# Optimization experiments

Hardware: AMD Instinct MI355X
Metric: run time of the kernel (lower is better)

The kernel has to match this reference:

```python
import jax, jax.numpy as jnp
import numpy as np

B, C, H, W = 2, 512, 64, 64
HEADS, DHEAD = 8, 64
HID = HEADS * DHEAD  # 512
GROUPS = 32
EPS = 1e-5


def setup_inputs() -> dict:
    key = jax.random.key(0)
    ks = jax.random.split(key, 10)
    w_scale = 0.02
    return {
        "x": jax.random.normal(ks[0], (B, C, H, W), dtype=jnp.float32),
        "gamma": jnp.ones((C,), dtype=jnp.float32),
        "beta": jnp.zeros((C,), dtype=jnp.float32),
        "wq": jax.random.normal(ks[1], (HID, C), dtype=jnp.float32) * w_scale,
        "bq": jax.random.normal(ks[2], (HID,), dtype=jnp.float32) * w_scale,
        "wk": jax.random.normal(ks[3], (HID, C), dtype=jnp.float32) * w_scale,
        "bk": jax.random.normal(ks[4], (HID,), dtype=jnp.float32) * w_scale,
        "wv": jax.random.normal(ks[5], (HID, C), dtype=jnp.float32) * w_scale,
        "bv": jax.random.normal(ks[6], (HID,), dtype=jnp.float32) * w_scale,
        "wo": jax.random.normal(ks[7], (C, HID), dtype=jnp.float32) * w_scale,
        "bo": jax.random.normal(ks[8], (C,), dtype=jnp.float32) * w_scale,
    }


def _group_norm(x, gamma, beta):
    b, c, h, w = x.shape
    xg = x.reshape(b, GROUPS, c // GROUPS, h * w)
    mu = jnp.mean(xg, axis=(2, 3), keepdims=True)
    var = jnp.var(xg, axis=(2, 3), keepdims=True)
    xn = (xg - mu) * jax.lax.rsqrt(var + EPS)
    xn = xn.reshape(b, c, h, w)
    return xn * gamma[None, :, None, None] + beta[None, :, None, None]


def reference(x, gamma, beta, wq, bq, wk, bk, wv, bv, wo, bo):
    b, c, h, w = x.shape
    n = h * w
    # norm + flatten spatial; embedding=None -> self-attention on normed x
    xn = _group_norm(x, gamma, beta).reshape(b, c, n)
    # 1x1 Conv1d projections == channel matmuls
    q = jnp.einsum('oc,bcn->bon', wq, xn) + bq[None, :, None]
    k = jnp.einsum('oc,bcn->bon', wk, xn) + bk[None, :, None]
    v = jnp.einsum('oc,bcn->bon', wv, xn) + bv[None, :, None]
    scale = DHEAD ** (-0.25)  # applied to BOTH q and k, as in source
    qh = q.reshape(b, HEADS, DHEAD, n) * scale
    kh = k.reshape(b, HEADS, DHEAD, n) * scale
    vh = v.reshape(b, HEADS, DHEAD, n)
    # full NxN attention (the materialized score matrix targeted for kernel work)
    attn = jax.nn.softmax(jnp.einsum('bhdi,bhdj->bhij', qh, kh), axis=-1)
    out = jnp.einsum('bhij,bhdj->bhdi', attn, vh).reshape(b, HID, n)
    out = jnp.einsum('oc,bcn->bon', wo, out) + bo[None, :, None]
    out = out.reshape(b, c, h, w)
    return x + out  # in_channels == out_channels -> residual
```

## Files before the change

kernel.cpp:

```cpp
#include <hip/hip_runtime.h>
#include <math.h>

#define BB      2
#define CC      512
#define NN_TOK  4096
#define HEADS   8
#define DHEAD   64
#define HID     512
#define GROUPS  32
#define CPG     (CC / GROUPS)
#define EPS     1e-5f

typedef __bf16 bf16x8 __attribute__((ext_vector_type(8)));
typedef float  f32x4  __attribute__((ext_vector_type(4)));
typedef float  f32x16 __attribute__((ext_vector_type(16)));
typedef int    i32x8  __attribute__((ext_vector_type(8)));

static __device__ __forceinline__ unsigned short f2bf(float f) {
  __bf16 h = (__bf16)f;
  return __builtin_bit_cast(unsigned short, h);
}
static __device__ __forceinline__ float bf2f(unsigned short u) {
  unsigned v = (unsigned)u << 16;
  return __builtin_bit_cast(float, v);
}
static __device__ __forceinline__ unsigned pk_fp8x4(float a, float b, float c, float d) {
  int lo = __builtin_amdgcn_cvt_pk_fp8_f32(a, b, 0, false);
  return (unsigned)__builtin_amdgcn_cvt_pk_fp8_f32(c, d, lo, true);
}
static __device__ __forceinline__ unsigned char f2fp8(float a) {
  return (unsigned char)(__builtin_amdgcn_cvt_pk_fp8_f32(a, a, 0, false) & 0xff);
}
static __device__ __forceinline__ float exp2_fast(float s) {
  float t = __builtin_fmaf(s, 8388608.0f, 1064993216.0f);
  int i = (int)t;
  return __builtin_bit_cast(float, i);
}
static __device__ __forceinline__ i32x8 ld_frag32(const unsigned char* p) {
  union { i32x8 v; long l[4]; } u;
  u.l[0] = *(const long*)(p + 0);
  u.l[1] = *(const long*)(p + 8);
  u.l[2] = *(const long*)(p + 16);
  u.l[3] = *(const long*)(p + 24);
  return u.v;
}
static __device__ __forceinline__ i32x8 ld_g32(const unsigned char* p) {
  union { i32x8 v; uint4 q[2]; } u;
  u.q[0] = *(const uint4*)(p);
  u.q[1] = *(const uint4*)(p + 16);
  return u.v;
}
#define SC_ONE 0x7F7F7F7F
#define QKV_WS 32.0f
#define QKV_WS_INV 0.03125f
#define WO_WS 16.0f
#define WO_WS_INV 0.0625f

__global__ __launch_bounds__(256) void gn_stats_wconv_kernel(
    const float* __restrict__ x, float2* __restrict__ part,
    const float* __restrict__ wq, const float* __restrict__ wk,
    const float* __restrict__ wv, const float* __restrict__ wo,
    unsigned char* __restrict__ wq8, unsigned char* __restrict__ wk8,
    unsigned char* __restrict__ wv8, unsigned char* __restrict__ wo8) {
  int blk = blockIdx.x;
  int t = threadIdx.x;
  {
    int wsel = blk >> 8;
    int off = (blk & 255) * 1024 + t * 4;
    const float* s = (wsel == 0) ? wq : (wsel == 1) ? wk : (wsel == 2) ? wv : wo;
    unsigned char* d = (wsel == 0) ? wq8 : (wsel == 1) ? wk8 : (wsel == 2) ? wv8 : wo8;
    float sc = (wsel < 3) ? QKV_WS : WO_WS;
    float4 a = *(const float4*)&s[off];
    *(unsigned*)&d[off] = pk_fp8x4(a.x * sc, a.y * sc, a.z * sc, a.w * sc);
  }
  const float4* __restrict__ x4 = (const float4*)(x + (size_t)blk * 4096);
  float s = 0.f, ss = 0.f;
  #pragma unroll
  for (int i = 0; i < 4; ++i) {
    float4 v = x4[t + i * 256];
    s  += v.x + v.y + v.z + v.w;
    ss += v.x * v.x + v.y * v.y + v.z * v.z + v.w * v.w;
  }
  #pragma unroll
  for (int off = 32; off >= 1; off >>= 1) {
    s  += __shfl_down(s, off, 64);
    ss += __shfl_down(ss, off, 64);
  }
  __shared__ float rs[4], rss[4];
  int wid = t >> 6, lane = t & 63;
  if (lane == 0) { rs[wid] = s; rss[wid] = ss; }
  __syncthreads();
  if (t == 0) {
    float2 o;
    o.x = rs[0] + rs[1] + rs[2] + rs[3];
    o.y = rss[0] + rss[1] + rss[2] + rss[3];
    part[blk] = o;
  }
}

__global__ __launch_bounds__(256) void gn_norm_t_kernel(
    const float* __restrict__ x, const float* __restrict__ gamma,
    const float* __restrict__ beta, const float2* __restrict__ part,
    unsigned char* __restrict__ xnT8) {
  __shared__ __align__(16) unsigned short lds[64 * 72];
  __shared__ float mu4[4], rs4[4];
  int b = blockIdx.z;
  int t0 = blockIdx.x * 64, c0 = blockIdx.y * 64;
  int t = threadIdx.x;
  if (t < 4) {
    int g = (c0 >> 4) + t;
    int gi = b * GROUPS + g;
    float S = 0.f, SS = 0.f;
    #pragma unroll
    for (int k = 0; k < 16; ++k) {
      float2 p = part[gi * 16 + k];
      S += p.x; SS += p.y;
    }
    const float inv_n = 1.0f / (float)(CPG * NN_TOK);
    float mu = S * inv_n;
    float var = SS * inv_n - mu * mu;
    mu4[t] = mu;
    rs4[t] = rsqrtf(var + EPS);
  }
  __syncthreads();
  const float* __restrict__ xb = x + (size_t)b * CC * NN_TOK;
  #pragma unroll
  for (int i = 0; i < 4; ++i) {
    int f = t + i * 256;
    int row = f >> 4, c16 = f & 15;
    int c = c0 + row;
    float ga = gamma[c] * rs4[row >> 4];
    float be = beta[c] - mu4[row >> 4] * ga;
    float4 v = *(const float4*)&xb[(size_t)c * NN_TOK + t0 + c16 * 4];
    ushort4 pk;
    pk.x = f2bf(v.x * ga + be); pk.y = f2bf(v.y * ga + be);
    pk.z = f2bf(v.z * ga + be); pk.w = f2bf(v.w * ga + be);
    *(ushort4*)&lds[row * 72 + c16 * 4] = pk;
  }
  __syncthreads();
  unsigned char* __restrict__ ob = xnT8 + (size_t)b * NN_TOK * CC;
  #pragma unroll
  for (int i = 0; i < 2; ++i) {
    int f = t + i * 256;
    int row = f >> 3, ch = f & 7;
    float v0 = bf2f(lds[(ch * 8 + 0) * 72 + row]);
    float v1 = bf2f(lds[(ch * 8 + 1) * 72 + row]);
    float v2 = bf2f(lds[(ch * 8 + 2) * 72 + row]);
    float v3 = bf2f(lds[(ch * 8 + 3) * 72 + row]);
    float v4 = bf2f(lds[(ch * 8 + 4) * 72 + row]);
    float v5 = bf2f(lds[(ch * 8 + 5) * 72 + row]);
    float v6 = bf2f(lds[(ch * 8 + 6) * 72 + row]);
    float v7 = bf2f(lds[(ch * 8 + 7) * 72 + row]);
    unsigned lo = pk_fp8x4(v0, v1, v2, v3);
    unsigned hi = pk_fp8x4(v4, v5, v6, v7);
    *(uint2*)&ob[(size_t)(t0 + row) * CC + c0 + ch * 8] = make_uint2(lo, hi);
  }
}

__global__ __launch_bounds__(256, 3) void qkv_gemm_kernel(
    const unsigned char* __restrict__ xnT8,
    const unsigned char* __restrict__ wq8, const unsigned char* __restrict__ wk8,
    const unsigned char* __restrict__ wv8,
    const float* __restrict__ bq, const float* __restrict__ bk,
    const float* __restrict__ bv,
    unsigned char* __restrict__ qT8, unsigned char* __restrict__ kT8,
    unsigned char* __restrict__ vB8) {
  __shared__ __align__(16) unsigned char AB[2][2][128 * 72];
  int b = blockIdx.z;
  int y = blockIdx.y;
  int which = y >> 2, yl = y & 3;
  const unsigned char* __restrict__ W =
      (which == 0) ? wq8 : (which == 1) ? wk8 : wv8;
  const float* __restrict__ bias = (which == 0) ? bq : (which == 1) ? bk : bv;
  int m0 = yl * 128;
  int n0 = blockIdx.x * 128;
  const unsigned char* __restrict__ Bsrc = xnT8 + (size_t)b * NN_TOK * CC;
  int t = threadIdx.x, w = t >> 6, lane = t & 63;
  int wm = (w >> 1) * 64, wn = (w & 1) * 64;
  int l31 = lane & 31, q1h = lane >> 5;

  int sr0 = t >> 2, sr1 = (t + 256) >> 2, sch = t & 3;
  const unsigned char* Wa0 = &W[(size_t)(m0 + sr0) * CC + sch * 16];
  const unsigned char* Wa1 = &W[(size_t)(m0 + sr1) * CC + sch * 16];
  const unsigned char* Bb0 = &Bsrc[(size_t)(n0 + sr0) * CC + sch * 16];
  const unsigned char* Bb1 = &Bsrc[(size_t)(n0 + sr1) * CC + sch * 16];
  uint4 ra0 = *(const uint4*)(Wa0);
  uint4 ra1 = *(const uint4*)(Wa1);
  uint4 rb0 = *(const uint4*)(Bb0);
  uint4 rb1 = *(const uint4*)(Bb1);

  const f32x16 z16 = {0,0,0,0,0,0,0,0,0,0,0,0,0,0,0,0};
  f32x16 acc[2][2];
  #pragma unroll
  for (int mt = 0; mt < 2; ++mt)
    #pragma unroll
    for (int nt = 0; nt < 2; ++nt) acc[mt][nt] = z16;

  int cur = 0;
  for (int kc = 0; kc < CC; kc += 64) {
    __syncthreads();
    {
      unsigned char* As = AB[cur][0];
      unsigned char* Bs = AB[cur][1];
      unsigned char* ad0 = &As[sr0 * 72 + sch * 16];
      *(uint2*)ad0 = make_uint2(ra0.x, ra0.y);
      *(uint2*)(ad0 + 8) = make_uint2(ra0.z, ra0.w);
      unsigned char* ad1 = &As[sr1 * 72 + sch * 16];
      *(uint2*)ad1 = make_uint2(ra1.x, ra1.y);
      *(uint2*)(ad1 + 8) = make_uint2(ra1.z, ra1.w);
      unsigned char* bd0 = &Bs[sr0 * 72 + sch * 16];
      *(uint2*)bd0 = make_uint2(rb0.x, rb0.y);
      *(uint2*)(bd0 + 8) = make_uint2(rb0.z, rb0.w);
      unsigned char* bd1 = &Bs[sr1 * 72 + sch * 16];
      *(uint2*)bd1 = make_uint2(rb1.x, rb1.y);
      *(uint2*)(bd1 + 8) = make_uint2(rb1.z, rb1.w);
    }
    if (kc + 64 < CC) {
      ra0 = *(const uint4*)(Wa0 + kc + 64);
      ra1 = *(const uint4*)(Wa1 + kc + 64);
      rb0 = *(const uint4*)(Bb0 + kc + 64);
      rb1 = *(const uint4*)(Bb1 + kc + 64);
    }
    __syncthreads();
    const unsigned char* As = AB[cur][0];
    const unsigned char* Bs = AB[cur][1];
    i32x8 af[2], bfm[2];
    #pragma unroll
    for (int i = 0; i < 2; ++i) {
      af[i]  = ld_frag32(&As[(wm + i * 32 + l31) * 72 + q1h * 32]);
      bfm[i] = ld_frag32(&Bs[(wn + i * 32 + l31) * 72 + q1h * 32]);
    }
    #pragma unroll
    for (int mt = 0; mt < 2; ++mt)
      #pragma unroll
      for (int nt = 0; nt < 2; ++nt)
        acc[mt][nt] = __builtin_amdgcn_mfma_scale_f32_32x32x64_f8f6f4(
            af[mt], bfm[nt], acc[mt][nt], 0, 0, 0, SC_ONE, 0, SC_ONE);
    cur ^= 1;
  }
  __syncthreads();

  if (which < 2) {
    const float sc = (which == 0) ? 0.18033688011112043f : 1.0f;
    unsigned char* __restrict__ dstT = (which == 0) ? qT8 : kT8;
    unsigned char* buf = (unsigned char*)AB + w * 2560;
    int h = (m0 + wm) >> 6;
    const size_t hbase = (size_t)(b * HEADS + h) * NN_TOK;
    #pragma unroll
    for (int p = 0; p < 2; ++p) {
      #pragma unroll
      for (int mt = 0; mt < 2; ++mt) {
        #pragma unroll
        for (int g = 0; g < 4; ++g) {
          float4 bv4 = *(const float4*)&bias[m0 + wm + mt * 32 + g * 8 + q1h * 4];
          f32x16 a = acc[mt][p];
          unsigned pk = pk_fp8x4((a[4 * g + 0] * QKV_WS_INV + bv4.x) * sc,
                                 (a[4 * g + 1] * QKV_WS_INV + bv4.y) * sc,
                                 (a[4 * g + 2] * QKV_WS_INV + bv4.z) * sc,
                                 (a[4 * g + 3] * QKV_WS_INV + bv4.w) * sc);
          *(unsigned*)&buf[l31 * 80 + mt * 32 + g * 8 + q1h * 4] = pk;
        }
      }
      #pragma unroll
      for (int it = 0; it < 2; ++it) {
        int idx = it * 64 + lane;
        int row = idx >> 2, ch = idx & 3;
        int tok = n0 + wn + p * 32 + row;
        *(uint4*)&dstT[(hbase + tok) * DHEAD + ch * 16] =
            *(const uint4*)&buf[row * 80 + ch * 16];
      }
      __syncthreads();
    }
  } else {
    unsigned char* __restrict__ dst = vB8 + (size_t)b * HID * NN_TOK;
    #pragma unroll
    for (int mt = 0; mt < 2; ++mt) {
      #pragma unroll
      for (int g = 0; g < 4; ++g) {
        float4 bv4 = *(const float4*)&bias[m0 + wm + mt * 32 + g * 8 + q1h * 4];
        float bvr[4] = {bv4.x, bv4.y, bv4.z, bv4.w};
        #pragma unroll
        for (int nt = 0; nt < 2; ++nt) {
          int tok = n0 + wn + nt * 32 + l31;
          #pragma unroll
          for (int r = 0; r < 4; ++r) {
            int m = m0 + wm + mt * 32 + g * 8 + q1h * 4 + r;
            dst[(size_t)m * NN_TOK + tok] =
                f2fp8(acc[mt][nt][4 * g + r] * QKV_WS_INV + bvr[r]);
          }
        }
      }
    }
  }
}

__global__ __launch_bounds__(256) void outproj_kernel(
    const unsigned char* __restrict__ aoT8, const unsigned char* __restrict__ wo8,
    const float* __restrict__ bo, const float* __restrict__ x,
    float* __restrict__ out) {
  __shared__ __align__(16) unsigned char As8[2][64 * 80];
  __shared__ __align__(16) unsigned char Bs8[2][64 * 80];
  int b = blockIdx.z;
  int m0 = blockIdx.y * 64;
  int n0 = blockIdx.x * 64;
  const unsigned char* __restrict__ Bsrc = aoT8 + (size_t)b * NN_TOK * HID;
  int t = threadIdx.x, w = t >> 6, lane = t & 63;
  int wm = (w & 1) * 32, wn = (w >> 1) * 32;
  int l31 = lane & 31, q1h = lane >> 5;

  int ar = t >> 2, ach = t & 3;
  const unsigned char* pa = &wo8[(size_t)(m0 + ar) * HID + ach * 16];
  const unsigned char* pbb = &Bsrc[(size_t)(n0 + ar) * HID + ach * 16];
  uint4 ra = *(const uint4*)(pa);
  uint4 rb = *(const uint4*)(pbb);

  const f32x16 z16 = {0,0,0,0,0,0,0,0,0,0,0,0,0,0,0,0};
  f32x16 acc = z16;

  int cur = 0;
  for (int kc = 0; kc < HID; kc += 64) {
    __syncthreads();
    *(uint4*)&As8[cur][ar * 80 + ach * 16] = ra;
    *(uint4*)&Bs8[cur][ar * 80 + ach * 16] = rb;
    if (kc + 64 < HID) {
      ra = *(const uint4*)(pa + kc + 64);
      rb = *(const uint4*)(pbb + kc + 64);
    }
    __syncthreads();
    i32x8 af = ld_frag32(&As8[cur][(wm + l31) * 80 + q1h * 32]);
    i32x8 bfm = ld_frag32(&Bs8[cur][(wn + l31) * 80 + q1h * 32]);
    acc = __builtin_amdgcn_mfma_scale_f32_32x32x64_f8f6f4(
        af, bfm, acc, 0, 0, 0, SC_ONE, 0, SC_ONE);
    cur ^= 1;
  }

  const float* __restrict__ xb = x + (size_t)b * CC * NN_TOK;
  float* __restrict__ ob = out + (size_t)b * CC * NN_TOK;
  int tok = n0 + wn + l31;
  #pragma unroll
  for (int g = 0; g < 4; ++g) {
    float4 bv4 = *(const float4*)&bo[m0 + wm + g * 8 + q1h * 4];
    float bvr[4] = {bv4.x, bv4.y, bv4.z, bv4.w};
    #pragma unroll
    for (int r = 0; r < 4; ++r) {
      int m = m0 + wm + g * 8 + q1h * 4 + r;
      size_t off = (size_t)m * NN_TOK + tok;
      ob[off] = acc[4 * g + r] * WO_WS_INV + bvr[r] + xb[off];
    }
  }
}

__global__ __launch_bounds__(512, 4) void attn_mfma_kernel(
    const unsigned char* __restrict__ qT8, const unsigned char* __restrict__ kT8,
    const unsigned char* __restrict__ vv8, unsigned char* __restrict__ aoT8) {
  __shared__ __align__(16) unsigned char kvs[2 * 9216];
  __shared__ __align__(16) unsigned char st8[4 * 32 * 80];
  __shared__ float lbuf[128];
  int bh = blockIdx.y;
  int b = bh >> 3, h = bh & 7;
  int i0 = blockIdx.x * 128;
  const size_t hb = (size_t)bh * NN_TOK;
  const unsigned char* __restrict__ qtg = qT8 + hb * DHEAD;
  const unsigned char* __restrict__ ktg = kT8 + hb * DHEAD;
  const unsigned char* __restrict__ vg  = vv8 + hb * DHEAD;
  int t = threadIdx.x;
  int w = t >> 6, lane = t & 63, l31 = lane & 31, q1h = lane >> 5;
  int strip = w & 3, parity = w >> 2;
  int iw = i0 + strip * 32;

  const unsigned char* qrow = qtg + (size_t)(iw + l31) * DHEAD + q1h * 32;
  uint4 qv0 = *(const uint4*)(qrow);
  uint4 qv1 = *(const uint4*)(qrow + 16);
  i32x8 qf = {(int)qv0.x, (int)qv0.y, (int)qv0.z, (int)qv0.w,
              (int)qv1.x, (int)qv1.y, (int)qv1.z, (int)qv1.w};
  i32x8 ones;
  #pragma unroll
  for (int i = 0; i < 8; ++i) ones[i] = 0x38383838;

  const unsigned char* kfb = ktg + (size_t)(parity * 64 + l31) * DHEAD + q1h * 32;

  int vtile = t >> 8, vrr = (t >> 2) & 63, vch = t & 3;
  const unsigned char* vga = &vg[(size_t)vrr * NN_TOK + vtile * 64 + vch * 16];
  int vbase = vtile * 4608 + vrr * 72 + 8 * (vch & 1) + 16 * (vch >> 1);

  uint4 vx = *(const uint4*)(vga);

  const f32x16 z16 = {0,0,0,0,0,0,0,0,0,0,0,0,0,0,0,0};
  f32x16 o0 = z16, o1 = z16, lacc = z16;

  int cur = 0;
  for (int rt = 0; rt < NN_TOK / 128; ++rt) {
    int j0 = rt * 128;
    {
      unsigned char* vd = kvs + cur * 9216 + vbase;
      *(uint2*)vd = make_uint2(vx.x, vx.z);
      *(uint2*)(vd + 32) = make_uint2(vx.y, vx.w);
    }
    if (rt + 1 < NN_TOK / 128)
      vx = *(const uint4*)(vga + (rt + 1) * 128);

    i32x8 ka0 = ld_g32(kfb + (size_t)j0 * DHEAD);
    i32x8 ka1 = ld_g32(kfb + (size_t)(j0 + 32) * DHEAD);

    __syncthreads();

    f32x16 s0 = __builtin_amdgcn_mfma_scale_f32_32x32x64_f8f6f4(
        ka0, qf, z16, 0, 0, 0, SC_ONE, 0, SC_ONE);
    f32x16 s1 = __builtin_amdgcn_mfma_scale_f32_32x32x64_f8f6f4(
        ka1, qf, z16, 0, 0, 0, SC_ONE, 0, SC_ONE);

    unsigned pk4[8];
    #pragma unroll
    for (int g = 0; g < 4; ++g) {
      float p0 = exp2_fast(s0[4 * g + 0]);
      float p1 = exp2_fast(s0[4 * g + 1]);
      float p2 = exp2_fast(s0[4 * g + 2]);
      float p3 = exp2_fast(s0[4 * g + 3]);
      pk4[g] = pk_fp8x4(p0, p1, p2, p3);
    }
    #pragma unroll
    for (int g = 0; g < 4; ++g) {
      float p0 = exp2_fast(s1[4 * g + 0]);
      float p1 = exp2_fast(s1[4 * g + 1]);
      float p2 = exp2_fast(s1[4 * g + 2]);
      float p3 = exp2_fast(s1[4 * g + 3]);
      pk4[4 + g] = pk_fp8x4(p0, p1, p2, p3);
    }

    i32x8 pb;
    #pragma unroll
    for (int g = 0; g < 8; ++g) pb[g] = (int)pk4[g];

    const unsigned char* vsw = kvs + cur * 9216 + parity * 4608;
    i32x8 va0 = ld_frag32(&vsw[l31 * 72 + q1h * 32]);
    i32x8 va1 = ld_frag32(&vsw[(32 + l31) * 72 + q1h * 32]);
    o0 = __builtin_amdgcn_mfma_scale_f32_32x32x64_f8f6f4(
        va0, pb, o0, 0, 0, 0, SC_ONE, 0, SC_ONE);
    o1 = __builtin_amdgcn_mfma_scale_f32_32x32x64_f8f6f4(
        va1, pb, o1, 0, 0, 0, SC_ONE, 0, SC_ONE);
    lacc = __builtin_amdgcn_mfma_scale_f32_32x32x64_f8f6f4(
        ones, pb, lacc, 0, 0, 0, SC_ONE, 0, SC_ONE);
    cur ^= 1;
  }
  float lrun = lacc[0];

  float* obuf = (float*)kvs;
  __syncthreads();
  if (parity == 1) {
    #pragma unroll
    for (int r = 0; r < 16; ++r) {
      int d = (r & 3) + 8 * (r >> 2) + 4 * q1h;
      obuf[strip * 1024 + d * 32 + l31] = o0[r];
    }
    if (q1h == 0) lbuf[strip * 32 + l31] = lrun;
  }
  __syncthreads();
  if (parity == 0) {
    lrun += lbuf[strip * 32 + l31];
    #pragma unroll
    for (int r = 0; r < 16; ++r) {
      int d = (r & 3) + 8 * (r >> 2) + 4 * q1h;
      o0[r] += obuf[strip * 1024 + d * 32 + l31];
    }
  }
  __syncthreads();
  if (parity == 1) {
    #pragma unroll
    for (int r = 0; r < 16; ++r) {
      int d = (r & 3) + 8 * (r >> 2) + 4 * q1h;
      obuf[strip * 1024 + d * 32 + l31] = o1[r];
    }
  }
  __syncthreads();
  if (parity == 0) {
    #pragma unroll
    for (int r = 0; r < 16; ++r) {
      int d = (r & 3) + 8 * (r >> 2) + 4 * q1h;
      o1[r] += obuf[strip * 1024 + d * 32 + l31];
    }
    float inv = 1.0f / lrun;
    unsigned char* stw = st8 + strip * 2560;
    #pragma unroll
    for (int dm = 0; dm < 2; ++dm) {
      #pragma unroll
      for (int g = 0; g < 4; ++g) {
        float v0 = ((dm == 0) ? o0[4 * g + 0] : o1[4 * g + 0]) * inv;
        float v1 = ((dm == 0) ? o0[4 * g + 1] : o1[4 * g + 1]) * inv;
        float v2 = ((dm == 0) ? o0[4 * g + 2] : o1[4 * g + 2]) * inv;
        float v3 = ((dm == 0) ? o0[4 * g + 3] : o1[4 * g + 3]) * inv;
        *(unsigned*)&stw[l31 * 80 + dm * 32 + g * 8 + q1h * 4] =
            pk_fp8x4(v0, v1, v2, v3);
      }
    }
    const size_t obase = (size_t)b * NN_TOK;
    #pragma unroll
    for (int it = 0; it < 4; ++it) {
      int idx = it * 64 + lane;
      int row = idx >> 3, ch = idx & 7;
      int tok = iw + row;
      *(uint2*)&aoT8[(obase + tok) * HID + h * DHEAD + ch * 8] =
          *(const uint2*)&stw[row * 80 + ch * 8];
    }
  }
}

extern "C" void kernel_launch(void* const* d_in, const int* in_sizes, int n_in,
                              void* d_out, int out_size, void* d_ws, size_t ws_size,
                              hipStream_t stream) {
  const float* x     = (const float*)d_in[0];
  const float* gamma = (const float*)d_in[1];
  const float* beta  = (const float*)d_in[2];
  const float* wq    = (const float*)d_in[3];
  const float* bq    = (const float*)d_in[4];
  const float* wk    = (const float*)d_in[5];
  const float* bk    = (const float*)d_in[6];
  const float* wv    = (const float*)d_in[7];
  const float* bv    = (const float*)d_in[8];
  const float* wo    = (const float*)d_in[9];
  const float* bo    = (const float*)d_in[10];
  float* out = (float*)d_out;

  const size_t SZ = (size_t)BB * CC * NN_TOK;
  const size_t WZ = (size_t)CC * HID;
  unsigned char* xnT8 = (unsigned char*)d_ws;
  unsigned char* qT8  = xnT8 + SZ;
  unsigned char* kT8  = qT8 + SZ;
  unsigned char* vB8  = kT8 + SZ;
  unsigned char* aoT8 = vB8 + SZ;
  unsigned char* wq8  = aoT8 + SZ;
  unsigned char* wk8  = wq8 + WZ;
  unsigned char* wv8  = wk8 + WZ;
  unsigned char* wo8  = wv8 + WZ;
  float2* gnpart = (float2*)(wo8 + WZ);

  gn_stats_wconv_kernel<<<dim3(1024), dim3(256), 0, stream>>>(
      x, gnpart, wq, wk, wv, wo, wq8, wk8, wv8, wo8);

  gn_norm_t_kernel<<<dim3(NN_TOK / 64, CC / 64, BB), dim3(256), 0, stream>>>(
      x, gamma, beta, gnpart, xnT8);

  qkv_gemm_kernel<<<dim3(NN_TOK / 128, 12, BB), dim3(256), 0, stream>>>(
      xnT8, wq8, wk8, wv8, bq, bk, bv, qT8, kT8, vB8);

  attn_mfma_kernel<<<dim3(NN_TOK / 128, BB * HEADS), dim3(512), 0, stream>>>(
      qT8, kT8, vB8, aoT8);

  outproj_kernel<<<dim3(NN_TOK / 64, CC / 64, BB), dim3(256), 0, stream>>>(
      aoT8, wo8, bo, x, out);
}
```

Measured before the change: 161.3 us.

## Pre-swizzle FP8 weights into MFMA fragment layout and load A directly from global

The weight conversion kernel now writes FP8 weights in a blocked layout of 32-row by 64-k tiles, matching the MFMA A-fragment order. The QKV and output-projection GEMMs then load A fragments straight from global memory with 32-byte loads instead of staging them through LDS. One __syncthreads per k-step is dropped and LDS use is roughly halved. In exchange, weight loads are unprefetched global reads on the critical path, and removing the leading barrier relies on the double buffering to keep the B-tile writes race-free.

```diff
diff --git a/kernel.cpp b/kernel.cpp
--- a/kernel.cpp
+++ b/kernel.cpp
@@ -55,6 +55,7 @@
 #define QKV_WS_INV 0.03125f
 #define WO_WS 16.0f
 #define WO_WS_INV 0.0625f
+
 
 __global__ __launch_bounds__(256) void gn_stats_wconv_kernel(
     const float* __restrict__ x, float2* __restrict__ part,
@@ -67,11 +68,13 @@
   {
     int wsel = blk >> 8;
     int off = (blk & 255) * 1024 + t * 4;
+    int m = off >> 9, k = off & 511;
+    int dst = (m >> 5) * 16384 + (k >> 6) * 2048 + (m & 31) * 64 + (k & 63);
     const float* s = (wsel == 0) ? wq : (wsel == 1) ? wk : (wsel == 2) ? wv : wo;
     unsigned char* d = (wsel == 0) ? wq8 : (wsel == 1) ? wk8 : (wsel == 2) ? wv8 : wo8;
     float sc = (wsel < 3) ? QKV_WS : WO_WS;
     float4 a = *(const float4*)&s[off];
-    *(unsigned*)&d[off] = pk_fp8x4(a.x * sc, a.y * sc, a.z * sc, a.w * sc);
+    *(unsigned*)&d[dst] = pk_fp8x4(a.x * sc, a.y * sc, a.z * sc, a.w * sc);
   }
   const float4* __restrict__ x4 = (const float4*)(x + (size_t)blk * 4096);
   float s = 0.f, ss = 0.f;
@@ -165,7 +168,7 @@
     const float* __restrict__ bv,
     unsigned char* __restrict__ qT8, unsigned char* __restrict__ kT8,
     unsigned char* __restrict__ vB8) {
-  __shared__ __align__(16) unsigned char AB[2][2][128 * 72];
+  __shared__ __align__(16) unsigned char Bs[2][128 * 72];
   int b = blockIdx.z;
   int y = blockIdx.y;
   int which = y >> 2, yl = y & 3;
@@ -179,13 +182,11 @@
   int wm = (w >> 1) * 64, wn = (w & 1) * 64;
   int l31 = lane & 31, q1h = lane >> 5;
 
+  const unsigned char* Wf = W + (size_t)(m0 + wm) * 512 + l31 * 64 + q1h * 32;
+
   int sr0 = t >> 2, sr1 = (t + 256) >> 2, sch = t & 3;
-  const unsigned char* Wa0 = &W[(size_t)(m0 + sr0) * CC + sch * 16];
-  const unsigned char* Wa1 = &W[(size_t)(m0 + sr1) * CC + sch * 16];
   const unsigned char* Bb0 = &Bsrc[(size_t)(n0 + sr0) * CC + sch * 16];
   const unsigned char* Bb1 = &Bsrc[(size_t)(n0 + sr1) * CC + sch * 16];
-  uint4 ra0 = *(const uint4*)(Wa0);
-  uint4 ra1 = *(const uint4*)(Wa1);
   uint4 rb0 = *(const uint4*)(Bb0);
   uint4 rb1 = *(const uint4*)(Bb1);
 
@@ -198,38 +199,28 @@
 
   int cur = 0;
   for (int kc = 0; kc < CC; kc += 64) {
-    __syncthreads();
     {
-      unsigned char* As = AB[cur][0];
-      unsigned char* Bs = AB[cur][1];
-      unsigned char* ad0 = &As[sr0 * 72 + sch * 16];
-      *(uint2*)ad0 = make_uint2(ra0.x, ra0.y);
-      *(uint2*)(ad0 + 8) = make_uint2(ra0.z, ra0.w);
-      unsigned char* ad1 = &As[sr1 * 72 + sch * 16];
-      *(uint2*)ad1 = make_uint2(ra1.x, ra1.y);
-      *(uint2*)(ad1 + 8) = make_uint2(ra1.z, ra1.w);
-      unsigned char* bd0 = &Bs[sr0 * 72 + sch * 16];
+      unsigned char* bd0 = &Bs[cur][sr0 * 72 + sch * 16];
       *(uint2*)bd0 = make_uint2(rb0.x, rb0.y);
       *(uint2*)(bd0 + 8) = make_uint2(rb0.z, rb0.w);
-      unsigned char* bd1 = &Bs[sr1 * 72 + sch * 16];
+      unsigned char* bd1 = &Bs[cur][sr1 * 72 + sch * 16];
       *(uint2*)bd1 = make_uint2(rb1.x, rb1.y);
       *(uint2*)(bd1 + 8) = make_uint2(rb1.z, rb1.w);
     }
     if (kc + 64 < CC) {
-      ra0 = *(const uint4*)(Wa0 + kc + 64);
-      ra1 = *(const uint4*)(Wa1 + kc + 64);
       rb0 = *(const uint4*)(Bb0 + kc + 64);
       rb1 = *(const uint4*)(Bb1 + kc + 64);
     }
+    i32x8 af[2];
+    #pragma unroll
+    for (int i = 0; i < 2; ++i)
+      af[i] = ld_g32(Wf + (size_t)i * 16384 + kc * 32);
+
     __syncthreads();
-    const unsigned char* As = AB[cur][0];
-    const unsigned char* Bs = AB[cur][1];
-    i32x8 af[2], bfm[2];
-    #pragma unroll
-    for (int i = 0; i < 2; ++i) {
-      af[i]  = ld_frag32(&As[(wm + i * 32 + l31) * 72 + q1h * 32]);
-      bfm[i] = ld_frag32(&Bs[(wn + i * 32 + l31) * 72 + q1h * 32]);
-    }
+    i32x8 bfm[2];
+    #pragma unroll
+    for (int i = 0; i < 2; ++i)
+      bfm[i] = ld_frag32(&Bs[cur][(wn + i * 32 + l31) * 72 + q1h * 32]);
     #pragma unroll
     for (int mt = 0; mt < 2; ++mt)
       #pragma unroll
@@ -243,7 +234,7 @@
   if (which < 2) {
     const float sc = (which == 0) ? 0.18033688011112043f : 1.0f;
     unsigned char* __restrict__ dstT = (which == 0) ? qT8 : kT8;
-    unsigned char* buf = (unsigned char*)AB + w * 2560;
+    unsigned char* buf = (unsigned char*)Bs + w * 2560;
     int h = (m0 + wm) >> 6;
     const size_t hbase = (size_t)(b * HEADS + h) * NN_TOK;
     #pragma unroll
@@ -298,7 +289,6 @@
     const unsigned char* __restrict__ aoT8, const unsigned char* __restrict__ wo8,
     const float* __restrict__ bo, const float* __restrict__ x,
     float* __restrict__ out) {
-  __shared__ __align__(16) unsigned char As8[2][64 * 80];
   __shared__ __align__(16) unsigned char Bs8[2][64 * 80];
   int b = blockIdx.z;
   int m0 = blockIdx.y * 64;
@@ -308,10 +298,10 @@
   int wm = (w & 1) * 32, wn = (w >> 1) * 32;
   int l31 = lane & 31, q1h = lane >> 5;
 
+  const unsigned char* Wf = wo8 + (size_t)(m0 + wm) * 512 + l31 * 64 + q1h * 32;
+
   int ar = t >> 2, ach = t & 3;
-  const unsigned char* pa = &wo8[(size_t)(m0 + ar) * HID + ach * 16];
   const unsigned char* pbb = &Bsrc[(size_t)(n0 + ar) * HID + ach * 16];
-  uint4 ra = *(const uint4*)(pa);
   uint4 rb = *(const uint4*)(pbb);
 
   const f32x16 z16 = {0,0,0,0,0,0,0,0,0,0,0,0,0,0,0,0};
@@ -319,15 +309,11 @@
 
   int cur = 0;
   for (int kc = 0; kc < HID; kc += 64) {
+    *(uint4*)&Bs8[cur][ar * 80 + ach * 16] = rb;
+    if (kc + 64 < HID)
+      rb = *(const uint4*)(pbb + kc + 64);
+    i32x8 af = ld_g32(Wf + kc * 32);
     __syncthreads();
-    *(uint4*)&As8[cur][ar * 80 + ach * 16] = ra;
-    *(uint4*)&Bs8[cur][ar * 80 + ach * 16] = rb;
-    if (kc + 64 < HID) {
-      ra = *(const uint4*)(pa + kc + 64);
-      rb = *(const uint4*)(pbb + kc + 64);
-    }
-    __syncthreads();
-    i32x8 af = ld_frag32(&As8[cur][(wm + l31) * 80 + q1h * 32]);
     i32x8 bfm = ld_frag32(&Bs8[cur][(wn + l31) * 80 + q1h * 32]);
     acc = __builtin_amdgcn_mfma_scale_f32_32x32x64_f8f6f4(
         af, bfm, acc, 0, 0, 0, SC_ONE, 0, SC_ONE);
```

New measurement: 164.3 us. No clear change (+1.9%).
